# Kernel tuning notes

Measured on AMD Instinct MI355X. Metric: run time of the kernel, lower is better.

## Reference

```python
import jax, jax.numpy as jnp
import numpy as np

NEG = -1e30  # effective -inf for log-space DP
EPS = 1e-7   # keras backend epsilon used by ctc_batch_cost


def setup_inputs() -> dict:
    key = jax.random.key(0)
    k1, k2 = jax.random.split(key)
    B, T, C, L = 256, 512, 256, 64
    y_true = jax.random.randint(k1, (B, L), 0, C - 1, dtype=jnp.int64)  # labels in [0, C-2]; blank = C-1
    y_pred = jax.random.uniform(k2, (B, T, C), dtype=jnp.float32)       # positive 'probabilities'
    return {"y_true": y_true, "y_pred": y_pred}


def _ctc_batch_cost(y_true, y_pred):
    # Faithful to tf.keras.backend.ctc_batch_cost with input_length=T, label_length=L
    # for every example, blank index = C-1, log applied as log(y_pred + eps).
    B, T, C = y_pred.shape
    L = y_true.shape[1]
    S = 2 * L + 1
    blank = C - 1
    logp = jnp.log(y_pred + EPS)                                  # [B, T, C]

    labels = y_true.astype(jnp.int32)
    # Extended label sequence: blank, l1, blank, l2, ..., lL, blank  -> [B, S]
    ext = jnp.full((B, S), blank, dtype=jnp.int32).at[:, 1::2].set(labels)
    # Skip transition (s-2 -> s) allowed iff s>=2, ext[s] != blank, ext[s] != ext[s-2]
    ext_m2 = jnp.concatenate([jnp.full((B, 2), blank, jnp.int32), ext[:, :-2]], axis=1)
    allow_skip = (jnp.arange(S)[None, :] >= 2) & (ext != blank) & (ext != ext_m2)  # [B, S]

    # Per-time log-probs of extended labels: [B, T, S]
    lp_ext = jnp.take_along_axis(logp, jnp.broadcast_to(ext[:, None, :], (B, T, S)), axis=2)

    # alpha init at t=0: only s=0 (blank) and s=1 (first label) are reachable
    alpha0 = jnp.where(jnp.arange(S)[None, :] < 2, lp_ext[:, 0, :], NEG)  # [B, S]
    neg1 = jnp.full((B, 1), NEG, y_pred.dtype)
    neg2 = jnp.full((B, 2), NEG, y_pred.dtype)

    def step(alpha, lp_t):
        a1 = jnp.concatenate([neg1, alpha[:, :-1]], axis=1)
        a2 = jnp.where(allow_skip, jnp.concatenate([neg2, alpha[:, :-2]], axis=1), NEG)
        m = jnp.maximum(alpha, jnp.maximum(a1, a2))
        new = m + jnp.log(jnp.exp(alpha - m) + jnp.exp(a1 - m) + jnp.exp(a2 - m)) + lp_t
        return new, None

    lp_seq = jnp.transpose(lp_ext[:, 1:, :], (1, 0, 2))            # [T-1, B, S]
    alphaT, _ = jax.lax.scan(step, alpha0, lp_seq)
    loss = -jnp.logaddexp(alphaT[:, S - 1], alphaT[:, S - 2])      # [B]
    return loss[:, None]                                           # [B, 1] like ctc_batch_cost


def reference(y_true, y_pred):
    # CTCLayer.call computes the loss (added via add_loss) and returns y_pred.
    # The loss is the meaningful computation; return it (per-example, [B, 1]).
    return _ctc_batch_cost(y_true, y_pred)
```

## Files before the change

### kernel.cpp

```cpp
#include <hip/hip_runtime.h>


constexpr int Bc = 256;
constexpr int Tc = 512;
constexpr int Cc = 256;
constexpr int Lc = 64;
constexpr int NS = 48;

#define EPSF (1e-7f)
#define NEGF (-1e30f)

__device__ __forceinline__ float flog2(float x) {
    float r; asm("v_log_f32 %0, %1" : "=v"(r) : "v"(x)); return r;
}
__device__ __forceinline__ float fexp2(float x) {
    float r; asm("v_exp_f32 %0, %1" : "=v"(r) : "v"(x)); return r;
}
__device__ __forceinline__ float lse2(float a, float b) {
    float m = fmaxf(a, b);
    float d = fminf(a, b) - m;
    return m + flog2(1.f + fexp2(d));
}
__device__ __forceinline__ float dlog2(double x) {
    if (!(x > 1e-300)) return NEGF;
    const int hb = __double2hiint(x);
    const int lb = __double2loint(x);
    const int e  = ((hb >> 20) & 0x7FF) - 1022;
    const double m = __hiloint2double((hb & 0x800FFFFF) | (1022 << 20), lb);
    return flog2((float)m) + (float)e;
}
__device__ __forceinline__ double dpp_up1_d(double old, double src) {
    const int rl = __builtin_amdgcn_update_dpp(
        __double2loint(old), __double2loint(src), 0x138, 0xF, 0xF, false);
    const int rh = __builtin_amdgcn_update_dpp(
        __double2hiint(old), __double2hiint(src), 0x138, 0xF, 0xF, false);
    return __hiloint2double(rh, rl);
}
__device__ __forceinline__ double dpp_dn1_d(double old, double src) {
    const int rl = __builtin_amdgcn_update_dpp(
        __double2loint(old), __double2loint(src), 0x130, 0xF, 0xF, false);
    const int rh = __builtin_amdgcn_update_dpp(
        __double2hiint(old), __double2hiint(src), 0x130, 0xF, 0xF, false);
    return __hiloint2double(rh, rl);
}
__device__ __forceinline__ void stage16(const float* g, float* l) {
    __builtin_amdgcn_global_load_lds(
        (const __attribute__((address_space(1))) void*)g,
        (__attribute__((address_space(3))) void*)l, 16, 0, 0);
}

__global__ __launch_bounds__(384, 1) void ctc_fb_kernel(
        const int* __restrict__ y_true,
        const float* __restrict__ y_pred,
        float* __restrict__ out)
{
    const int b    = blockIdx.x;
    const int lane = threadIdx.x & 63;
    const int wid  = threadIdx.x >> 6;

    __shared__ float ring[2][NS][Cc];
    __shared__ float Cl[64], Ch[64];
    __shared__ float CexS;

    const float* __restrict__ bbase = y_pred + (size_t)b * Tc * Cc;

    double lo = 0.0, hi = 0.0, ex = 0.0;

    if (wid >= 2) {
        const int pid  = wid - 2;
        const int dir  = pid & 1;
        const int half = pid >> 1;
        const float* __restrict__ g0 =
            dir ? (bbase + (size_t)(Tc - 1) * Cc + lane * 4)
                : (bbase + lane * 4);
        const ptrdiff_t stp = dir ? -(ptrdiff_t)Cc : (ptrdiff_t)Cc;
        float* const lds0 = &ring[dir][0][0];
        #pragma unroll
        for (int G = 0; G < 4; ++G) {
            #pragma unroll
            for (int j = 0; j < 4; ++j) {
                const int u = 8 * G + 4 * half + j;
                stage16(g0 + stp * u, lds0 + u * Cc);
            }
        }
        int sg = 32;
        for (int g = 0; g < 32; ++g) {
            if (g <= 27) {
                const float* gb = g0 + stp * (8 * (g + 4) + 4 * half);
                float* lb = lds0 + (sg + 4 * half) * Cc;
                #pragma unroll
                for (int j = 0; j < 4; ++j)
                    stage16(gb + stp * j, lb + j * Cc);
            }
            if (g <= 27)      asm volatile("s_waitcnt vmcnt(16)" ::: "memory");
            else if (g == 28) asm volatile("s_waitcnt vmcnt(12)" ::: "memory");
            else if (g == 29) asm volatile("s_waitcnt vmcnt(8)"  ::: "memory");
            else if (g == 30) asm volatile("s_waitcnt vmcnt(4)"  ::: "memory");
            else              asm volatile("s_waitcnt vmcnt(0)"  ::: "memory");
            __builtin_amdgcn_s_barrier();
            sg += 8; if (sg >= NS) sg = 0;
        }
    } else {
        const int lab  = y_true[b * Lc + lane];
        const int labp = __shfl_up(lab, 1);
        const int labn = __shfl_down(lab, 1);

        if (wid == 0) {
            const bool allowF = (lane >= 1) && (lab != labp);
            auto stepF = [&](float pBf, float pLf) {
                const double pB = (double)pBf, pL = (double)pLf;
                const double prevHi = dpp_up1_d(0.0, hi);
                const double sk  = allowF ? prevHi : 0.0;
                const double nlo = (lo + prevHi) * pB;
                const double nhi = (hi + lo + sk) * pL;
                ex = (ex + hi) * pB;
                hi = nhi; lo = nlo;
            };
            int sb = 0;
            for (int g = 0; g < 32; ++g) {
                asm volatile("" ::: "memory");
                __builtin_amdgcn_s_barrier();
                asm volatile("" ::: "memory");
#define RDF(j) const float cL##j = ring[0][sb + j][lab] + EPSF, \
                           cB##j = ring[0][sb + j][Cc - 1] + EPSF;
                RDF(0) RDF(1) RDF(2) RDF(3) RDF(4) RDF(5) RDF(6) RDF(7)
#undef RDF
                if (g == 0) {
                    lo = (lane == 0) ? (double)cB0 : 0.0;
                    hi = (lane == 0) ? (double)cL0 : 0.0;
                } else stepF(cB0, cL0);
                stepF(cB1, cL1); stepF(cB2, cL2); stepF(cB3, cL3);
                stepF(cB4, cL4); stepF(cB5, cL5); stepF(cB6, cL6);
                stepF(cB7, cL7);
                sb += 8; if (sb >= NS) sb = 0;
            }
        } else {
            const bool allowB = (lane < 63) && (labn != lab);
            auto stepB = [&](float pBf, float pLf) {
                const double pB = (double)pBf, pL = (double)pLf;
                const double nlo_s = dpp_dn1_d(ex, lo);
                const double nhi_s = dpp_dn1_d(0.0, hi);
                const double sk = allowB ? nhi_s : 0.0;
                const double l2 = (lo + hi) * pB;
                const double h2 = (hi + nlo_s + sk) * pL;
                ex = ex * pB;
                lo = l2; hi = h2;
            };
            int sb = 0;
            for (int g = 0; g < 32; ++g) {
                asm volatile("" ::: "memory");
                __builtin_amdgcn_s_barrier();
                asm volatile("" ::: "memory");
#define RDB(j) const float cL##j = ring[1][sb + j][lab] + EPSF, \
                           cB##j = ring[1][sb + j][Cc - 1] + EPSF;
                RDB(0) RDB(1) RDB(2) RDB(3) RDB(4) RDB(5) RDB(6) RDB(7)
#undef RDB
                if (g == 0) {
                    ex = (double)cB0;
                    hi = (lane == 63) ? (double)cL0 : 0.0;
                    lo = 0.0;
                } else stepB(cB0, cL0);
                stepB(cB1, cL1); stepB(cB2, cL2); stepB(cB3, cL3);
                stepB(cB4, cL4); stepB(cB5, cL5); stepB(cB6, cL6);
                stepB(cB7, cL7);
                sb += 8; if (sb >= NS) sb = 0;
            }
            const double nlo_s = dpp_dn1_d(ex, lo);
            const double nhi_s = dpp_dn1_d(0.0, hi);
            const double sk = allowB ? nhi_s : 0.0;
            Cl[lane] = dlog2(lo + hi);
            Ch[lane] = dlog2(hi + nlo_s + sk);
            if (lane == 63) CexS = dlog2(ex);
        }
    }

    __syncthreads();

    if (wid == 0) {
        const float w1 = dlog2(lo) + Cl[lane];
        const float w2 = dlog2(hi) + Ch[lane];
        float w = lse2(w1, w2);
        if (lane == 63) w = lse2(w, dlog2(ex) + CexS);
        #pragma unroll
        for (int off = 32; off; off >>= 1) w = lse2(w, __shfl_xor(w, off));
        if (lane == 0)
            out[b] = -0.69314718055994530942f * w;
    }
}

extern "C" void kernel_launch(void* const* d_in, const int* in_sizes, int n_in,
                              void* d_out, int out_size, void* d_ws, size_t ws_size,
                              hipStream_t stream) {
    const int*   y_true = (const int*)d_in[0];
    const float* y_pred = (const float*)d_in[1];
    float*       out    = (float*)d_out;
    ctc_fb_kernel<<<dim3(Bc), dim3(384), 0, stream>>>(y_true, y_pred, out);
}
```

Baseline: 26.42 us.

## Stage producer loads through registers instead of direct global-to-LDS loads

The producer waves stop using global_load_lds and instead load float4 rows into registers, then write them into the LDS ring. The loop is double-buffered with two register sets and a barrier after each group write. This avoids the direct-to-LDS load path, but it cuts the number of global loads in flight from about four groups to two. It also adds VGPR traffic and lgkmcnt waits on a kernel that appears to be bandwidth-bound.

```diff
diff --git a/kernel.cpp b/kernel.cpp
--- a/kernel.cpp
+++ b/kernel.cpp
@@ -42,11 +42,6 @@
     const int rh = __builtin_amdgcn_update_dpp(
         __double2hiint(old), __double2hiint(src), 0x130, 0xF, 0xF, false);
     return __hiloint2double(rh, rl);
-}
-__device__ __forceinline__ void stage16(const float* g, float* l) {
-    __builtin_amdgcn_global_load_lds(
-        (const __attribute__((address_space(1))) void*)g,
-        (__attribute__((address_space(3))) void*)l, 16, 0, 0);
 }
 
 __global__ __launch_bounds__(384, 1) void ctc_fb_kernel(
@@ -74,32 +69,52 @@
             dir ? (bbase + (size_t)(Tc - 1) * Cc + lane * 4)
                 : (bbase + lane * 4);
         const ptrdiff_t stp = dir ? -(ptrdiff_t)Cc : (ptrdiff_t)Cc;
-        float* const lds0 = &ring[dir][0][0];
-        #pragma unroll
-        for (int G = 0; G < 4; ++G) {
-            #pragma unroll
-            for (int j = 0; j < 4; ++j) {
-                const int u = 8 * G + 4 * half + j;
-                stage16(g0 + stp * u, lds0 + u * Cc);
+
+        float4 a0, a1, a2, a3, b0, b1, b2, b3;
+
+#define GADDR(G, j) (g0 + stp * (8 * (G) + 4 * half + (j)))
+#define LADDR(G, j) (&ring[dir][((G) % 6) * 8 + 4 * half + (j)][lane * 4])
+#define PLOAD(v0, v1, v2, v3, G)                                   \
+        v0 = *(const float4*)GADDR(G, 0);                          \
+        v1 = *(const float4*)GADDR(G, 1);                          \
+        v2 = *(const float4*)GADDR(G, 2);                          \
+        v3 = *(const float4*)GADDR(G, 3);
+#define PWRITE(v0, v1, v2, v3, G)                                  \
+        *(float4*)LADDR(G, 0) = v0;                                \
+        *(float4*)LADDR(G, 1) = v1;                                \
+        *(float4*)LADDR(G, 2) = v2;                                \
+        *(float4*)LADDR(G, 3) = v3;
+
+        PLOAD(a0, a1, a2, a3, 0)
+        PLOAD(b0, b1, b2, b3, 1)
+        asm volatile("s_waitcnt vmcnt(4)" ::: "memory");
+        PWRITE(a0, a1, a2, a3, 0)
+        asm volatile("s_waitcnt lgkmcnt(0)" ::: "memory");
+
+        for (int g = 0; g < 32; g += 2) {
+            asm volatile("" ::: "memory");
+            __builtin_amdgcn_s_barrier();
+            asm volatile("" ::: "memory");
+            if (g + 2 <= 31) { PLOAD(a0, a1, a2, a3, g + 2) }
+            if (g <= 29) asm volatile("s_waitcnt vmcnt(4)" ::: "memory");
+            else         asm volatile("s_waitcnt vmcnt(0)" ::: "memory");
+            PWRITE(b0, b1, b2, b3, g + 1)
+            asm volatile("s_waitcnt lgkmcnt(0)" ::: "memory");
+            asm volatile("" ::: "memory");
+            __builtin_amdgcn_s_barrier();
+            asm volatile("" ::: "memory");
+            if (g + 3 <= 31) { PLOAD(b0, b1, b2, b3, g + 3) }
+            if (g + 1 <= 29) asm volatile("s_waitcnt vmcnt(4)" ::: "memory");
+            else             asm volatile("s_waitcnt vmcnt(0)" ::: "memory");
+            if (g + 2 <= 31) {
+                PWRITE(a0, a1, a2, a3, g + 2)
+                asm volatile("s_waitcnt lgkmcnt(0)" ::: "memory");
             }
         }
-        int sg = 32;
-        for (int g = 0; g < 32; ++g) {
-            if (g <= 27) {
-                const float* gb = g0 + stp * (8 * (g + 4) + 4 * half);
-                float* lb = lds0 + (sg + 4 * half) * Cc;
-                #pragma unroll
-                for (int j = 0; j < 4; ++j)
-                    stage16(gb + stp * j, lb + j * Cc);
-            }
-            if (g <= 27)      asm volatile("s_waitcnt vmcnt(16)" ::: "memory");
-            else if (g == 28) asm volatile("s_waitcnt vmcnt(12)" ::: "memory");
-            else if (g == 29) asm volatile("s_waitcnt vmcnt(8)"  ::: "memory");
-            else if (g == 30) asm volatile("s_waitcnt vmcnt(4)"  ::: "memory");
-            else              asm volatile("s_waitcnt vmcnt(0)"  ::: "memory");
-            __builtin_amdgcn_s_barrier();
-            sg += 8; if (sg >= NS) sg = 0;
-        }
+#undef GADDR
+#undef LADDR
+#undef PLOAD
+#undef PWRITE
     } else {
         const int lab  = y_true[b * Lc + lane];
         const int labp = __shfl_up(lab, 1);
```

New measurement: 25.29 us. -4.2%, faster.
